# Optimization experiments

Measured on AMD Instinct MI355X. Metric: run time of the kernel, lower is better.

## Reference

```python
import jax, jax.numpy as jnp
import numpy as np

NUM_ITERATIONS = 3
LN_EPS = 1e-5


def setup_inputs() -> dict:
    key = jax.random.key(0)
    ks = jax.random.split(key, 10)
    B, L, Lv, H = 8, 2048, 256, 1024
    s = 1.0 / np.sqrt(H)
    s2 = 1.0 / np.sqrt(2 * H)
    return {
        "text_feat": jax.random.normal(ks[0], (B, L, H), dtype=jnp.float32),
        "vision_feat": jax.random.normal(ks[1], (B, Lv, H), dtype=jnp.float32),
        "Wt": jax.random.uniform(ks[2], (H, H), jnp.float32, -s, s),
        "bt": jax.random.uniform(ks[3], (H,), jnp.float32, -s, s),
        "Wv": jax.random.uniform(ks[4], (H, H), jnp.float32, -s, s),
        "bv": jax.random.uniform(ks[5], (H,), jnp.float32, -s, s),
        "Wg": jax.random.uniform(ks[6], (H, 2 * H), jnp.float32, -s2, s2),
        "bg": jax.random.uniform(ks[7], (H,), jnp.float32, -s2, s2),
        "gamma": jnp.ones((H,), jnp.float32),
        "beta": jnp.zeros((H,), jnp.float32),
    }


def reference(text_feat, vision_feat, Wt, bt, Wv, bv, Wg, bg, gamma, beta):
    B, L, H = text_feat.shape
    # mean-pool vision over its sequence, broadcast over L
    vision_pooled = jnp.mean(vision_feat, axis=1, keepdims=True)          # [B,1,H]
    text_proj = jnp.einsum('blh,oh->blo', text_feat, Wt) + bt             # [B,L,H]
    vision_proj = jnp.einsum('bkh,oh->bko', vision_pooled, Wv) + bv       # [B,1,H]
    vision_proj = jnp.broadcast_to(vision_proj, (B, L, H))                # expand to [B,L,H]

    # agreement is loop-invariant in the original code; compute once
    agreement = jnp.sum(text_proj * vision_proj, axis=-1, keepdims=True)  # [B,L,1]

    coupling = jnp.zeros((B, L, 1), dtype=text_feat.dtype)
    fused = text_feat
    for _ in range(NUM_ITERATIONS):
        routing_weights = jax.nn.softmax(coupling, axis=1)                # softmax over L
        weighted_vision = routing_weights * vision_proj                   # [B,L,H]
        # gate = sigmoid(Linear(concat(text_proj, weighted_vision)))
        Wg_t, Wg_v = Wg[:, :H], Wg[:, H:]
        gate_pre = (jnp.einsum('blh,oh->blo', text_proj, Wg_t)
                    + jnp.einsum('blh,oh->blo', weighted_vision, Wg_v) + bg)
        gate = jax.nn.sigmoid(gate_pre)
        fused = text_feat + gate * weighted_vision
        coupling = coupling + agreement

    # LayerNorm over last dim (dropout is identity in eval)
    mu = jnp.mean(fused, axis=-1, keepdims=True)
    var = jnp.mean(jnp.square(fused - mu), axis=-1, keepdims=True)
    out = (fused - mu) / jnp.sqrt(var + LN_EPS) * gamma + beta
    return out
```

## Files before the change

### kernel.cpp

```cpp
#include <hip/hip_runtime.h>
#include <hip/hip_bf16.h>
#include <hip/hip_fp8.h>

typedef __bf16 bf16_t;
typedef bf16_t bf16x4 __attribute__((ext_vector_type(4)));
typedef bf16_t bf16x8 __attribute__((ext_vector_type(8)));
typedef float  f32x4  __attribute__((ext_vector_type(4)));

#define B_  8
#define L_  2048
#define H_  1024
#define LV_ 256

typedef const __attribute__((address_space(1))) void* gptr_as1;
typedef __attribute__((address_space(3))) void* lptr_as3;

__device__ __forceinline__ void gload_lds16(void* lds_base, const void* gsrc) {
  __builtin_amdgcn_global_load_lds((gptr_as1)gsrc, (lptr_as3)lds_base, 16, 0, 0);
}

__device__ __forceinline__ unsigned char to_fp8(float x) {
  return __hip_fp8_e4m3(x).__x;
}

__global__ __launch_bounds__(256) void prep1(const float* __restrict__ vf,
                                             const float* __restrict__ Wt,
                                             const float* __restrict__ Wg,
                                             const float* __restrict__ bt,
                                             const float* __restrict__ bg,
                                             float* __restrict__ pooled,
                                             bf16_t* __restrict__ WtT,
                                             float* __restrict__ cbb,
                                             float* __restrict__ u) {
  __shared__ __align__(16) char shm[16640];
  int bid = blockIdx.x;
  int t = threadIdx.x;
  if (bid < 64) {
    float* part = (float*)shm;
    int b = bid >> 3, hc = bid & 7;
    int h = hc * 128 + (t & 127);
    int kh = t >> 7;
    const float* p = vf + (long)b * (LV_ * H_) + (long)kh * 128 * H_ + h;
    float s = 0.f;
    #pragma unroll 4
    for (int k = 0; k < 128; ++k) s += p[k * H_];
    part[t] = s;
    __syncthreads();
    if (t < 128)
      pooled[b * H_ + hc * 128 + t] = (part[t] + part[t + 128]) * (1.f / 256.f);
  } else if (bid < 320) {
    float (*tile)[65] = (float(*)[65])shm;
    int lb = bid - 64;
    int hr = (lb >> 4) * 64;
    int ec = (lb & 15) * 64;
    int lr = t >> 4, lc = t & 15;
    #pragma unroll
    for (int rr = 0; rr < 4; ++rr) {
      int r = rr * 16 + lr;
      float4 v = *(const float4*)(Wt + (long)(hr + r) * H_ + ec + lc * 4);
      tile[r][lc * 4 + 0] = v.x; tile[r][lc * 4 + 1] = v.y;
      tile[r][lc * 4 + 2] = v.z; tile[r][lc * 4 + 3] = v.w;
    }
    __syncthreads();
    #pragma unroll
    for (int rr = 0; rr < 4; ++rr) {
      int er = rr * 16 + lr;
      bf16x4 o = { (bf16_t)tile[lc * 4 + 0][er], (bf16_t)tile[lc * 4 + 1][er],
                   (bf16_t)tile[lc * 4 + 2][er], (bf16_t)tile[lc * 4 + 3][er] };
      *(bf16x4*)(WtT + (long)(ec + er) * H_ + hr + lc * 4) = o;
    }
  } else if (bid < 576) {
    int lb = bid - 320;
    int wid = t >> 6, lane = t & 63;
    int o = lb * 4 + wid;
    const float* wr = Wg + (long)o * 2048;
    float acc = 0.f;
    for (int j = 0; j < 16; ++j) acc += wr[lane + 64 * j] * bt[lane + 64 * j];
    for (int off = 32; off; off >>= 1) acc += __shfl_down(acc, off);
    if (lane == 0) cbb[o] = acc + bg[o];
  } else {
    int z = bid - 576;
    *(float4*)(u + z * 1024 + t * 4) = (float4){0.f, 0.f, 0.f, 0.f};
  }
}

__global__ void matvec8(const float* __restrict__ W, int ldw, int woff,
                        const float* __restrict__ x,
                        const float* __restrict__ bias,
                        float* __restrict__ out) {
  int wid = threadIdx.x >> 6, lane = threadIdx.x & 63;
  int o = blockIdx.x * 4 + wid;
  const float* wr = W + (long)o * ldw + woff;
  float acc[B_];
  #pragma unroll
  for (int b = 0; b < B_; ++b) acc[b] = 0.f;
  for (int j = 0; j < 16; ++j) {
    float w = wr[lane + 64 * j];
    #pragma unroll
    for (int b = 0; b < B_; ++b) acc[b] += w * x[b * H_ + lane + 64 * j];
  }
  #pragma unroll
  for (int b = 0; b < B_; ++b)
    for (int off = 32; off; off >>= 1) acc[b] += __shfl_down(acc[b], off);
  if (lane == 0) {
    float bb = bias ? bias[o] : 0.f;
    #pragma unroll
    for (int b = 0; b < B_; ++b) out[b * H_ + o] = acc[b] + bb;
  }
}

__global__ __launch_bounds__(256) void prep3(const float* __restrict__ Wg,
                                             const float* __restrict__ Wt,
                                             const float* __restrict__ vp,
                                             float* __restrict__ gv,
                                             float* __restrict__ u) {
  int bid = blockIdx.x;
  int t = threadIdx.x;
  if (bid < 256) {
    int wid = t >> 6, lane = t & 63;
    int o = bid * 4 + wid;
    const float* wr = Wg + (long)o * 2048 + 1024;
    float acc[B_];
    #pragma unroll
    for (int b = 0; b < B_; ++b) acc[b] = 0.f;
    for (int j = 0; j < 16; ++j) {
      float w = wr[lane + 64 * j];
      #pragma unroll
      for (int b = 0; b < B_; ++b) acc[b] += w * vp[b * H_ + lane + 64 * j];
    }
    #pragma unroll
    for (int b = 0; b < B_; ++b)
      for (int off = 32; off; off >>= 1) acc[b] += __shfl_down(acc[b], off);
    if (lane == 0) {
      #pragma unroll
      for (int b = 0; b < B_; ++b) gv[b * H_ + o] = acc[b];
    }
  } else {
    int lb = bid - 256;
    int e = (lb & 3) * 256 + t;
    int oc = lb >> 2;
    float a[B_];
    #pragma unroll
    for (int b = 0; b < B_; ++b) a[b] = 0.f;
    #pragma unroll
    for (int i = 0; i < 16; ++i) {
      int o = oc * 16 + i;
      float w = Wt[(long)o * H_ + e];
      #pragma unroll
      for (int b = 0; b < B_; ++b) a[b] += w * vp[b * H_ + o];
    }
    #pragma unroll
    for (int b = 0; b < B_; ++b) atomicAdd(u + b * 1024 + e, a[b]);
  }
}

__global__ __launch_bounds__(256) void cvt_wc(const float* __restrict__ text,
                                              const float* __restrict__ u,
                                              const float* __restrict__ Wg,
                                              const bf16_t* __restrict__ Bt,
                                              unsigned char* __restrict__ t8p,
                                              float* __restrict__ agr,
                                              unsigned char* __restrict__ Cw8) {
  __shared__ __align__(16) char shm[32800];
  int bid = blockIdx.x;
  int t = threadIdx.x;
  if (bid < 1024) {
    unsigned char (*q8)[1032] = (unsigned char(*)[1032])shm;
    float (*dred)[16] = (float(*)[16])(shm + 16512);
    int b = bid >> 7;
    int wid = t >> 6, lane = t & 63;
    const float4* trow = (const float4*)(text + (long)bid * (16 * H_));
    float4 uu = ((const float4*)(u + b * H_))[t];
    #pragma unroll 4
    for (int i = 0; i < 16; ++i) {
      float4 v = trow[i * 256 + t];
      float d = v.x * uu.x + v.y * uu.y + v.z * uu.z + v.w * uu.w;
      for (int off = 32; off; off >>= 1) d += __shfl_down(d, off);
      if (!lane) dred[wid][i] = d;
      uchar4 q = { to_fp8(v.x), to_fp8(v.y), to_fp8(v.z), to_fp8(v.w) };
      *(uchar4*)&q8[i][t * 4] = q;
    }
    __syncthreads();
    if (t < 16)
      agr[bid * 16 + t] = dred[0][t] + dred[1][t] + dred[2][t] + dred[3][t];
    unsigned char* dst = t8p + (long)(bid >> 2) * 65536 + (bid & 3) * 512;
    #pragma unroll
    for (int c = 0; c < 8; ++c) {
      int kb = wid * 8 + c;
      uint2 r = *(const uint2*)&q8[lane & 15][kb * 32 + (lane >> 4) * 8];
      *(uint2*)(dst + kb * 2048 + lane * 8) = r;
    }
    return;
  }
  const int tid = t;
  const int wid = tid >> 6, lane = tid & 63;
  const int fr = lane & 15, fkb = (lane >> 4) * 16, fq = (lane >> 4) * 4;
  const int wm = wid >> 1, wn = wid & 1;
  const int lb = bid - 1024;
  const int tm = lb & 15, tn = lb >> 4;
  const int m0 = tm * 64, n0 = tn * 64;

  char* ldsA = shm;

  const int d0 = tid * 16;
  const int p  = d0 ^ (((d0 >> 7) & 7) << 4);
  const int rS = p >> 7, cS = (p & 127) >> 1;

  const int swz = (fr & 7) << 4;
  const int e0 = fkb ^ swz;
  const int e1 = (64 + fkb) ^ swz;

  auto stage = [&](int tt) {
    char* base = ldsA + (tt & 1) * 16384;
    gload_lds16(base + 8192 + d0,        Bt + (long)(n0 + rS) * H_ + tt * 64 + cS);
    gload_lds16(base + 8192 + 4096 + d0, Bt + (long)(n0 + 32 + rS) * H_ + tt * 64 + cS);
    const float* a0 = Wg + (long)(m0 + rS) * 2048 + tt * 64 + cS;
    const float* a1 = Wg + (long)(m0 + 32 + rS) * 2048 + tt * 64 + cS;
    float4 x0 = *(const float4*)a0, x1 = *(const float4*)(a0 + 4);
    float4 y0 = *(const float4*)a1, y1 = *(const float4*)(a1 + 4);
    bf16x8 bx = { (bf16_t)x0.x, (bf16_t)x0.y, (bf16_t)x0.z, (bf16_t)x0.w,
                  (bf16_t)x1.x, (bf16_t)x1.y, (bf16_t)x1.z, (bf16_t)x1.w };
    bf16x8 by = { (bf16_t)y0.x, (bf16_t)y0.y, (bf16_t)y0.z, (bf16_t)y0.w,
                  (bf16_t)y1.x, (bf16_t)y1.y, (bf16_t)y1.z, (bf16_t)y1.w };
    *(bf16x8*)(base + d0) = bx;
    *(bf16x8*)(base + 4096 + d0) = by;
  };

  f32x4 acc[2][2];
  #pragma unroll
  for (int m = 0; m < 2; ++m)
    #pragma unroll
    for (int n = 0; n < 2; ++n) acc[m][n] = (f32x4){0.f, 0.f, 0.f, 0.f};

  stage(0);
  __syncthreads();
  for (int tt = 0; tt < 16; ++tt) {
    if (tt + 1 < 16) stage(tt + 1);
    char* buf = ldsA + (tt & 1) * 16384;
    char* AR = buf + (wm * 32 + fr) * 128;
    char* BR = buf + 8192 + (wn * 32 + fr) * 128;
    bf16x8 a[2][2], b[2][2];
    #pragma unroll
    for (int m = 0; m < 2; ++m) {
      a[m][0] = *(const bf16x8*)(AR + m * 2048 + e0);
      a[m][1] = *(const bf16x8*)(AR + m * 2048 + e1);
      b[m][0] = *(const bf16x8*)(BR + m * 2048 + e0);
      b[m][1] = *(const bf16x8*)(BR + m * 2048 + e1);
    }
    #pragma unroll
    for (int m = 0; m < 2; ++m)
      #pragma unroll
      for (int n = 0; n < 2; ++n) {
        acc[m][n] = __builtin_amdgcn_mfma_f32_16x16x32_bf16(a[m][0], b[n][0], acc[m][n], 0, 0, 0);
        acc[m][n] = __builtin_amdgcn_mfma_f32_16x16x32_bf16(a[m][1], b[n][1], acc[m][n], 0, 0, 0);
      }
    __syncthreads();
  }
  #pragma unroll
  for (int m = 0; m < 2; ++m)
    #pragma unroll
    for (int r_ = 0; r_ < 4; ++r_) {
      int row = m0 + wm * 32 + m * 16 + fq + r_;
      #pragma unroll
      for (int n = 0; n < 2; ++n) {
        int col = n0 + wn * 32 + n * 16 + fr;
        Cw8[(long)(row >> 7) * 131072 + (col >> 5) * 4096 + ((row >> 4) & 7) * 512
            + ((row & 15) + (((col >> 3) & 3) << 4)) * 8 + (col & 7)]
          = to_fp8(acc[m][n][r_] * 16.f);
      }
    }
}

#define BOFF 16777216
__global__ __launch_bounds__(512, 2)
void gemm_ln(const unsigned char* __restrict__ AB,
             const float* __restrict__ textf,
             const float* __restrict__ cbb, const float* __restrict__ agrb,
             const float* __restrict__ gvb, const float* __restrict__ vpb,
             const float* __restrict__ gamma, const float* __restrict__ beta,
             float* __restrict__ out) {
  extern __shared__ __align__(16) char dlds[];
  const int tid  = threadIdx.x;
  const int w    = tid >> 6;
  const int lane = tid & 63;
  const int fr   = lane & 15;
  const int fq   = (lane >> 4) * 4;
  const int bid  = blockIdx.x;
  const long m0  = (long)bid * 64;
  const int bat  = (int)(m0 >> 11);

  {
    float* red = (float*)(dlds + 118784);
    float* rvA = (float*)(dlds + 118848);
    float4 av = *(const float4*)(agrb + (long)bat * 2048 + tid * 4);
    float mloc = fmaxf(fmaxf(av.x, av.y), fmaxf(av.z, av.w)) * 2.f;
    #pragma unroll
    for (int off = 32; off; off >>= 1) mloc = fmaxf(mloc, __shfl_xor(mloc, off));
    if ((tid & 63) == 0) red[tid >> 6] = mloc;
    __syncthreads();
    float mx = red[0];
    #pragma unroll
    for (int i = 1; i < 8; ++i) mx = fmaxf(mx, red[i]);
    float sl = __expf(2.f * av.x - mx) + __expf(2.f * av.y - mx)
             + __expf(2.f * av.z - mx) + __expf(2.f * av.w - mx);
    #pragma unroll
    for (int off = 32; off; off >>= 1) sl += __shfl_xor(sl, off);
    __syncthreads();
    if ((tid & 63) == 0) red[tid >> 6] = sl;
    __syncthreads();
    float ssum = red[0] + red[1] + red[2] + red[3]
               + red[4] + red[5] + red[6] + red[7];
    if (tid < 64) rvA[tid] = __expf(2.f * agrb[m0 + tid] - mx) / ssum;
    __syncthreads();
  }

  {
    char* P = dlds + 98304;
    if (tid < 256) {
      gload_lds16(P + tid * 16,          cbb + tid * 4);
      gload_lds16(P + 8192 + tid * 16,   vpb + bat * H_ + tid * 4);
      gload_lds16(P + 16384 + tid * 16,  beta + tid * 4);
    } else {
      int t2 = tid - 256;
      gload_lds16(P + 4096 + t2 * 16,    gvb + bat * H_ + t2 * 4);
      gload_lds16(P + 12288 + t2 * 16,   gamma + t2 * 4);
    }
  }

  const unsigned char* aSrc = AB + (long)bid * 65536 + lane * 16;
  const unsigned char* bSrc = AB + BOFF + (long)w * 131072 + lane * 16;
  char* const wBase = dlds + w * 12288;

  f32x4 acc[4][8];
  #pragma unroll
  for (int m = 0; m < 4; ++m)
    #pragma unroll
    for (int n = 0; n < 8; ++n) acc[m][n] = (f32x4){0.f, 0.f, 0.f, 0.f};

#define STAGE(t)                                                        \
  {                                                                     \
    char* D_ = wBase + ((t) & 1) * 6144 + lane * 16;                    \
    const unsigned char* As_ = aSrc + (t) * 2048;                       \
    gload_lds16(D_,        As_);                                        \
    gload_lds16(D_ + 1024, As_ + 1024);                                 \
    const unsigned char* Bs_ = bSrc + (t) * 4096;                       \
    _Pragma("unroll")                                                   \
    for (int r_ = 0; r_ < 4; ++r_)                                      \
      gload_lds16(D_ + 2048 + r_ * 1024, Bs_ + r_ * 1024);              \
  }
#define KITER(t, WN)                                                    \
  {                                                                     \
    asm volatile("s_waitcnt lgkmcnt(0)" ::: "memory");                  \
    __builtin_amdgcn_sched_barrier(0);                                  \
    if ((t) + 1 < 32) STAGE((t) + 1)                                    \
    asm volatile("s_waitcnt vmcnt(" #WN ")" ::: "memory");              \
    __builtin_amdgcn_sched_barrier(0);                                  \
    const char* R_ = wBase + ((t) & 1) * 6144 + lane * 8;               \
    long a_[4], b_[8];                                                  \
    _Pragma("unroll")                                                   \
    for (int m_ = 0; m_ < 4; ++m_)                                      \
      a_[m_] = *(const long*)(R_ + m_ * 512);                           \
    _Pragma("unroll")                                                   \
    for (int n_ = 0; n_ < 8; ++n_)                                      \
      b_[n_] = *(const long*)(R_ + 2048 + n_ * 512);                    \
    _Pragma("unroll")                                                   \
    for (int m_ = 0; m_ < 4; ++m_)                                      \
      _Pragma("unroll")                                                 \
      for (int n_ = 0; n_ < 8; ++n_)                                    \
        acc[m_][n_] = __builtin_amdgcn_mfma_f32_16x16x32_fp8_fp8(       \
            a_[m_], b_[n_], acc[m_][n_], 0, 0, 0);                      \
  }

  STAGE(0)

  KITER(0, 6)  KITER(1, 6)  KITER(2, 6)  KITER(3, 6)
  KITER(4, 6)  KITER(5, 6)  KITER(6, 6)  KITER(7, 6)
  KITER(8, 6)  KITER(9, 6)  KITER(10, 6) KITER(11, 6)
  KITER(12, 6) KITER(13, 6) KITER(14, 6) KITER(15, 6)
  KITER(16, 6) KITER(17, 6) KITER(18, 6) KITER(19, 6)
  KITER(20, 6) KITER(21, 6) KITER(22, 6) KITER(23, 6)
  KITER(24, 6) KITER(25, 6) KITER(26, 6) KITER(27, 6)
  KITER(28, 6) KITER(29, 6) KITER(30, 6) KITER(31, 0)
#undef KITER
#undef STAGE

  const int lr = tid >> 5;
  const int jj = tid & 31;
  char* P = dlds + 98304;
  const float* rvA = (const float*)(dlds + 118848);

  #pragma unroll
  for (int m = 0; m < 4; ++m) {
    __syncthreads();
    #pragma unroll
    for (int n = 0; n < 8; ++n) {
      #pragma unroll
      for (int r = 0; r < 4; ++r) {
        int rl = fq + r;
        int c  = (w * 128 + n * 16 + fr) ^ (((rl >> 2) & 3) << 4);
        *(float*)(dlds + rl * 4096 + c * 4) = acc[m][n][r];
      }
    }
    __syncthreads();
    long row = m0 + m * 16 + lr;
    float rv = rvA[m * 16 + lr];
    const float* tf = textf + row * H_;
    const int rot = ((lr >> 2) & 3) << 4;
    float s = 0.f, q = 0.f;
    #pragma unroll 2
    for (int k = 0; k < 8; ++k) {
      int c0 = k * 128 + jj * 4;
      char* slot = dlds + lr * 4096 + ((c0 ^ rot) * 4);
      f32x4 a4 = *(const f32x4*)slot;
      float4 t4  = *(const float4*)(tf + c0);
      f32x4 cb4 = *(const f32x4*)(P + c0 * 4);
      f32x4 gv4 = *(const f32x4*)(P + 4096 + c0 * 4);
      f32x4 vp4 = *(const f32x4*)(P + 8192 + c0 * 4);
      f32x4 f4;
      float gp, g;
      gp = a4[0] * 0.0625f + cb4[0] + rv * gv4[0];
      g = 1.f / (1.f + __expf(-gp));
      f4[0] = t4.x + g * rv * vp4[0];
      gp = a4[1] * 0.0625f + cb4[1] + rv * gv4[1];
      g = 1.f / (1.f + __expf(-gp));
      f4[1] = t4.y + g * rv * vp4[1];
      gp = a4[2] * 0.0625f + cb4[2] + rv * gv4[2];
      g = 1.f / (1.f + __expf(-gp));
      f4[2] = t4.z + g * rv * vp4[2];
      gp = a4[3] * 0.0625f + cb4[3] + rv * gv4[3];
      g = 1.f / (1.f + __expf(-gp));
      f4[3] = t4.w + g * rv * vp4[3];
      *(f32x4*)slot = f4;
      s += f4[0] + f4[1] + f4[2] + f4[3];
      q += f4[0] * f4[0] + f4[1] * f4[1] + f4[2] * f4[2] + f4[3] * f4[3];
    }
    #pragma unroll
    for (int off = 1; off < 32; off <<= 1) {
      s += __shfl_xor(s, off);
      q += __shfl_xor(q, off);
    }
    float mu  = s * (1.f / H_);
    float var = q * (1.f / H_) - mu * mu;
    float inv = rsqrtf(var + 1e-5f);
    float* op = out + row * H_;
    #pragma unroll 2
    for (int k = 0; k < 8; ++k) {
      int c0 = k * 128 + jj * 4;
      f32x4 f4 = *(const f32x4*)(dlds + lr * 4096 + ((c0 ^ rot) * 4));
      f32x4 gg = *(const f32x4*)(P + 12288 + c0 * 4);
      f32x4 bb = *(const f32x4*)(P + 16384 + c0 * 4);
      float4 o4;
      o4.x = (f4[0] - mu) * inv * gg[0] + bb[0];
      o4.y = (f4[1] - mu) * inv * gg[1] + bb[1];
      o4.z = (f4[2] - mu) * inv * gg[2] + bb[2];
      o4.w = (f4[3] - mu) * inv * gg[3] + bb[3];
      *(float4*)(op + c0) = o4;
    }
  }
}

extern "C" void kernel_launch(void* const* d_in, const int* in_sizes, int n_in,
                              void* d_out, int out_size, void* d_ws, size_t ws_size,
                              hipStream_t stream) {
  const float* text  = (const float*)d_in[0];
  const float* vis   = (const float*)d_in[1];
  const float* Wt    = (const float*)d_in[2];
  const float* bt    = (const float*)d_in[3];
  const float* Wv    = (const float*)d_in[4];
  const float* bv    = (const float*)d_in[5];
  const float* Wg    = (const float*)d_in[6];
  const float* bg    = (const float*)d_in[7];
  const float* gamma = (const float*)d_in[8];
  const float* beta  = (const float*)d_in[9];
  float* out = (float*)d_out;

  char* ws = (char*)d_ws;
  unsigned char* t8p   = (unsigned char*)(ws);
  unsigned char* Wc8p  = (unsigned char*)(ws + (size_t)16777216);
  bf16_t* WtT_b = (bf16_t*)(ws + (size_t)17825792);
  float*  pooled = (float*)(ws + (size_t)19922944);
  float*  vp     = (float*)(ws + (size_t)19955712);
  float*  gv     = (float*)(ws + (size_t)19988480);
  float*  u      = (float*)(ws + (size_t)20021248);
  float*  cbb    = (float*)(ws + (size_t)20054016);
  float*  agr    = (float*)(ws + (size_t)20123648);

  static bool smem_set = false;
  if (!smem_set) {
    (void)hipFuncSetAttribute((const void*)gemm_ln,
                              hipFuncAttributeMaxDynamicSharedMemorySize, 119296);
    smem_set = true;
  }

  prep1<<<584, 256, 0, stream>>>(vis, Wt, Wg, bt, bg, pooled, WtT_b, cbb, u);
  matvec8<<<256, 256, 0, stream>>>(Wv, 1024, 0, pooled, bv, vp);
  prep3<<<512, 256, 0, stream>>>(Wg, Wt, vp, gv, u);
  cvt_wc<<<1280, 256, 0, stream>>>(text, u, Wg, WtT_b, t8p, agr, Wc8p);
  gemm_ln<<<256, 512, 119296, stream>>>(t8p, text, cbb, agr, gv, vp,
                                        gamma, beta, out);
}
```

Baseline: 98.89 us.

## Merge four prep kernels into one persistent kernel with grid barriers

New measurement: 313.1 us. 3.17x slower.

```diff
diff --git a/kernel.cpp b/kernel.cpp
--- a/kernel.cpp
+++ b/kernel.cpp
@@ -23,18 +23,33 @@
   return __hip_fp8_e4m3(x).__x;
 }
 
-__global__ __launch_bounds__(256) void prep1(const float* __restrict__ vf,
-                                             const float* __restrict__ Wt,
-                                             const float* __restrict__ Wg,
-                                             const float* __restrict__ bt,
-                                             const float* __restrict__ bg,
-                                             float* __restrict__ pooled,
-                                             bf16_t* __restrict__ WtT,
-                                             float* __restrict__ cbb,
-                                             float* __restrict__ u) {
-  __shared__ __align__(16) char shm[16640];
-  int bid = blockIdx.x;
-  int t = threadIdx.x;
+__device__ __forceinline__ void grid_bar(unsigned int* bar, unsigned int target) {
+  __syncthreads();
+  if (threadIdx.x == 0) {
+    __threadfence();
+    atomicAdd(bar, 1u);
+    while (__hip_atomic_load(bar, __ATOMIC_RELAXED, __HIP_MEMORY_SCOPE_AGENT)
+           < target)
+      __builtin_amdgcn_s_sleep(8);
+    __threadfence();
+  }
+  __syncthreads();
+}
+
+__global__ __launch_bounds__(256, 4)
+void mega_prep(const float* __restrict__ vf, const float* __restrict__ Wt,
+               const float* __restrict__ Wg, const float* __restrict__ bt,
+               const float* __restrict__ bg, const float* __restrict__ bv,
+               const float* __restrict__ Wv, const float* __restrict__ text,
+               float* __restrict__ pooled, bf16_t* __restrict__ WtT,
+               float* __restrict__ cbb, float* __restrict__ u,
+               float* __restrict__ vp, float* __restrict__ gv,
+               unsigned char* __restrict__ t8p, float* __restrict__ agr,
+               unsigned char* __restrict__ Cw8, unsigned int* __restrict__ bar) {
+  __shared__ __align__(16) char shm[33024];
+  const int bid = blockIdx.x;
+  const int t = threadIdx.x;
+
   if (bid < 64) {
     float* part = (float*)shm;
     int b = bid >> 3, hc = bid & 7;
@@ -78,44 +93,35 @@
     for (int j = 0; j < 16; ++j) acc += wr[lane + 64 * j] * bt[lane + 64 * j];
     for (int off = 32; off; off >>= 1) acc += __shfl_down(acc, off);
     if (lane == 0) cbb[o] = acc + bg[o];
-  } else {
+  } else if (bid < 584) {
     int z = bid - 576;
     *(float4*)(u + z * 1024 + t * 4) = (float4){0.f, 0.f, 0.f, 0.f};
   }
-}
-
-__global__ void matvec8(const float* __restrict__ W, int ldw, int woff,
-                        const float* __restrict__ x,
-                        const float* __restrict__ bias,
-                        float* __restrict__ out) {
-  int wid = threadIdx.x >> 6, lane = threadIdx.x & 63;
-  int o = blockIdx.x * 4 + wid;
-  const float* wr = W + (long)o * ldw + woff;
-  float acc[B_];
-  #pragma unroll
-  for (int b = 0; b < B_; ++b) acc[b] = 0.f;
-  for (int j = 0; j < 16; ++j) {
-    float w = wr[lane + 64 * j];
-    #pragma unroll
-    for (int b = 0; b < B_; ++b) acc[b] += w * x[b * H_ + lane + 64 * j];
-  }
-  #pragma unroll
-  for (int b = 0; b < B_; ++b)
-    for (int off = 32; off; off >>= 1) acc[b] += __shfl_down(acc[b], off);
-  if (lane == 0) {
-    float bb = bias ? bias[o] : 0.f;
-    #pragma unroll
-    for (int b = 0; b < B_; ++b) out[b * H_ + o] = acc[b] + bb;
-  }
-}
-
-__global__ __launch_bounds__(256) void prep3(const float* __restrict__ Wg,
-                                             const float* __restrict__ Wt,
-                                             const float* __restrict__ vp,
-                                             float* __restrict__ gv,
-                                             float* __restrict__ u) {
-  int bid = blockIdx.x;
-  int t = threadIdx.x;
+  grid_bar(bar, 768);
+
+  if (bid < 256) {
+    int wid = t >> 6, lane = t & 63;
+    int o = bid * 4 + wid;
+    const float* wr = Wv + (long)o * H_;
+    float acc[B_];
+    #pragma unroll
+    for (int b = 0; b < B_; ++b) acc[b] = 0.f;
+    for (int j = 0; j < 16; ++j) {
+      float w = wr[lane + 64 * j];
+      #pragma unroll
+      for (int b = 0; b < B_; ++b) acc[b] += w * pooled[b * H_ + lane + 64 * j];
+    }
+    #pragma unroll
+    for (int b = 0; b < B_; ++b)
+      for (int off = 32; off; off >>= 1) acc[b] += __shfl_down(acc[b], off);
+    if (lane == 0) {
+      float bb = bv[o];
+      #pragma unroll
+      for (int b = 0; b < B_; ++b) vp[b * H_ + o] = acc[b] + bb;
+    }
+  }
+  grid_bar(bar, 1536);
+
   if (bid < 256) {
     int wid = t >> 6, lane = t & 63;
     int o = bid * 4 + wid;
@@ -135,7 +141,7 @@
       #pragma unroll
       for (int b = 0; b < B_; ++b) gv[b * H_ + o] = acc[b];
     }
-  } else {
+  } else if (bid < 512) {
     int lb = bid - 256;
     int e = (lb & 3) * 256 + t;
     int oc = lb >> 2;
@@ -152,123 +158,115 @@
     #pragma unroll
     for (int b = 0; b < B_; ++b) atomicAdd(u + b * 1024 + e, a[b]);
   }
-}
-
-__global__ __launch_bounds__(256) void cvt_wc(const float* __restrict__ text,
-                                              const float* __restrict__ u,
-                                              const float* __restrict__ Wg,
-                                              const bf16_t* __restrict__ Bt,
-                                              unsigned char* __restrict__ t8p,
-                                              float* __restrict__ agr,
-                                              unsigned char* __restrict__ Cw8) {
-  __shared__ __align__(16) char shm[32800];
-  int bid = blockIdx.x;
-  int t = threadIdx.x;
-  if (bid < 1024) {
-    unsigned char (*q8)[1032] = (unsigned char(*)[1032])shm;
-    float (*dred)[16] = (float(*)[16])(shm + 16512);
-    int b = bid >> 7;
-    int wid = t >> 6, lane = t & 63;
-    const float4* trow = (const float4*)(text + (long)bid * (16 * H_));
-    float4 uu = ((const float4*)(u + b * H_))[t];
-    #pragma unroll 4
-    for (int i = 0; i < 16; ++i) {
-      float4 v = trow[i * 256 + t];
-      float d = v.x * uu.x + v.y * uu.y + v.z * uu.z + v.w * uu.w;
-      for (int off = 32; off; off >>= 1) d += __shfl_down(d, off);
-      if (!lane) dred[wid][i] = d;
-      uchar4 q = { to_fp8(v.x), to_fp8(v.y), to_fp8(v.z), to_fp8(v.w) };
-      *(uchar4*)&q8[i][t * 4] = q;
-    }
-    __syncthreads();
-    if (t < 16)
-      agr[bid * 16 + t] = dred[0][t] + dred[1][t] + dred[2][t] + dred[3][t];
-    unsigned char* dst = t8p + (long)(bid >> 2) * 65536 + (bid & 3) * 512;
-    #pragma unroll
-    for (int c = 0; c < 8; ++c) {
-      int kb = wid * 8 + c;
-      uint2 r = *(const uint2*)&q8[lane & 15][kb * 32 + (lane >> 4) * 8];
-      *(uint2*)(dst + kb * 2048 + lane * 8) = r;
-    }
-    return;
-  }
-  const int tid = t;
-  const int wid = tid >> 6, lane = tid & 63;
-  const int fr = lane & 15, fkb = (lane >> 4) * 16, fq = (lane >> 4) * 4;
-  const int wm = wid >> 1, wn = wid & 1;
-  const int lb = bid - 1024;
-  const int tm = lb & 15, tn = lb >> 4;
-  const int m0 = tm * 64, n0 = tn * 64;
-
-  char* ldsA = shm;
-
-  const int d0 = tid * 16;
-  const int p  = d0 ^ (((d0 >> 7) & 7) << 4);
-  const int rS = p >> 7, cS = (p & 127) >> 1;
-
-  const int swz = (fr & 7) << 4;
-  const int e0 = fkb ^ swz;
-  const int e1 = (64 + fkb) ^ swz;
-
-  auto stage = [&](int tt) {
-    char* base = ldsA + (tt & 1) * 16384;
-    gload_lds16(base + 8192 + d0,        Bt + (long)(n0 + rS) * H_ + tt * 64 + cS);
-    gload_lds16(base + 8192 + 4096 + d0, Bt + (long)(n0 + 32 + rS) * H_ + tt * 64 + cS);
-    const float* a0 = Wg + (long)(m0 + rS) * 2048 + tt * 64 + cS;
-    const float* a1 = Wg + (long)(m0 + 32 + rS) * 2048 + tt * 64 + cS;
-    float4 x0 = *(const float4*)a0, x1 = *(const float4*)(a0 + 4);
-    float4 y0 = *(const float4*)a1, y1 = *(const float4*)(a1 + 4);
-    bf16x8 bx = { (bf16_t)x0.x, (bf16_t)x0.y, (bf16_t)x0.z, (bf16_t)x0.w,
-                  (bf16_t)x1.x, (bf16_t)x1.y, (bf16_t)x1.z, (bf16_t)x1.w };
-    bf16x8 by = { (bf16_t)y0.x, (bf16_t)y0.y, (bf16_t)y0.z, (bf16_t)y0.w,
-                  (bf16_t)y1.x, (bf16_t)y1.y, (bf16_t)y1.z, (bf16_t)y1.w };
-    *(bf16x8*)(base + d0) = bx;
-    *(bf16x8*)(base + 4096 + d0) = by;
-  };
-
-  f32x4 acc[2][2];
-  #pragma unroll
-  for (int m = 0; m < 2; ++m)
-    #pragma unroll
-    for (int n = 0; n < 2; ++n) acc[m][n] = (f32x4){0.f, 0.f, 0.f, 0.f};
-
-  stage(0);
-  __syncthreads();
-  for (int tt = 0; tt < 16; ++tt) {
-    if (tt + 1 < 16) stage(tt + 1);
-    char* buf = ldsA + (tt & 1) * 16384;
-    char* AR = buf + (wm * 32 + fr) * 128;
-    char* BR = buf + 8192 + (wn * 32 + fr) * 128;
-    bf16x8 a[2][2], b[2][2];
-    #pragma unroll
-    for (int m = 0; m < 2; ++m) {
-      a[m][0] = *(const bf16x8*)(AR + m * 2048 + e0);
-      a[m][1] = *(const bf16x8*)(AR + m * 2048 + e1);
-      b[m][0] = *(const bf16x8*)(BR + m * 2048 + e0);
-      b[m][1] = *(const bf16x8*)(BR + m * 2048 + e1);
-    }
-    #pragma unroll
-    for (int m = 0; m < 2; ++m)
-      #pragma unroll
-      for (int n = 0; n < 2; ++n) {
-        acc[m][n] = __builtin_amdgcn_mfma_f32_16x16x32_bf16(a[m][0], b[n][0], acc[m][n], 0, 0, 0);
-        acc[m][n] = __builtin_amdgcn_mfma_f32_16x16x32_bf16(a[m][1], b[n][1], acc[m][n], 0, 0, 0);
+  grid_bar(bar, 2304);
+
+  for (int u_ = bid; u_ < 1280; u_ += 768) {
+    if (u_ < 256) {
+      const int tid = t;
+      const int wid = tid >> 6, lane = tid & 63;
+      const int fr = lane & 15, fkb = (lane >> 4) * 16, fq = (lane >> 4) * 4;
+      const int wm = wid >> 1, wn = wid & 1;
+      const int tm = u_ & 15, tn = u_ >> 4;
+      const int m0 = tm * 64, n0 = tn * 64;
+      char* ldsA = shm;
+      const int d0 = tid * 16;
+      const int p  = d0 ^ (((d0 >> 7) & 7) << 4);
+      const int rS = p >> 7, cS = (p & 127) >> 1;
+      const int swz = (fr & 7) << 4;
+      const int e0 = fkb ^ swz;
+      const int e1 = (64 + fkb) ^ swz;
+
+      auto stage = [&](int tt) {
+        char* base = ldsA + (tt & 1) * 16384;
+        gload_lds16(base + 8192 + d0,        WtT + (long)(n0 + rS) * H_ + tt * 64 + cS);
+        gload_lds16(base + 8192 + 4096 + d0, WtT + (long)(n0 + 32 + rS) * H_ + tt * 64 + cS);
+        const float* a0 = Wg + (long)(m0 + rS) * 2048 + tt * 64 + cS;
+        const float* a1 = Wg + (long)(m0 + 32 + rS) * 2048 + tt * 64 + cS;
+        float4 x0 = *(const float4*)a0, x1 = *(const float4*)(a0 + 4);
+        float4 y0 = *(const float4*)a1, y1 = *(const float4*)(a1 + 4);
+        bf16x8 bx = { (bf16_t)x0.x, (bf16_t)x0.y, (bf16_t)x0.z, (bf16_t)x0.w,
+                      (bf16_t)x1.x, (bf16_t)x1.y, (bf16_t)x1.z, (bf16_t)x1.w };
+        bf16x8 by = { (bf16_t)y0.x, (bf16_t)y0.y, (bf16_t)y0.z, (bf16_t)y0.w,
+                      (bf16_t)y1.x, (bf16_t)y1.y, (bf16_t)y1.z, (bf16_t)y1.w };
+        *(bf16x8*)(base + d0) = bx;
+        *(bf16x8*)(base + 4096 + d0) = by;
+      };
+
+      f32x4 acc[2][2];
+      #pragma unroll
+      for (int m = 0; m < 2; ++m)
+        #pragma unroll
+        for (int n = 0; n < 2; ++n) acc[m][n] = (f32x4){0.f, 0.f, 0.f, 0.f};
+
+      stage(0);
+      __syncthreads();
+      for (int tt = 0; tt < 16; ++tt) {
+        if (tt + 1 < 16) stage(tt + 1);
+        char* buf = ldsA + (tt & 1) * 16384;
+        char* AR = buf + (wm * 32 + fr) * 128;
+        char* BR = buf + 8192 + (wn * 32 + fr) * 128;
+        bf16x8 a[2][2], b[2][2];
+        #pragma unroll
+        for (int m = 0; m < 2; ++m) {
+          a[m][0] = *(const bf16x8*)(AR + m * 2048 + e0);
+          a[m][1] = *(const bf16x8*)(AR + m * 2048 + e1);
+          b[m][0] = *(const bf16x8*)(BR + m * 2048 + e0);
+          b[m][1] = *(const bf16x8*)(BR + m * 2048 + e1);
+        }
+        #pragma unroll
+        for (int m = 0; m < 2; ++m)
+          #pragma unroll
+          for (int n = 0; n < 2; ++n) {
+            acc[m][n] = __builtin_amdgcn_mfma_f32_16x16x32_bf16(a[m][0], b[n][0], acc[m][n], 0, 0, 0);
+            acc[m][n] = __builtin_amdgcn_mfma_f32_16x16x32_bf16(a[m][1], b[n][1], acc[m][n], 0, 0, 0);
+          }
+        __syncthreads();
       }
-    __syncthreads();
-  }
-  #pragma unroll
-  for (int m = 0; m < 2; ++m)
-    #pragma unroll
-    for (int r_ = 0; r_ < 4; ++r_) {
-      int row = m0 + wm * 32 + m * 16 + fq + r_;
-      #pragma unroll
-      for (int n = 0; n < 2; ++n) {
-        int col = n0 + wn * 32 + n * 16 + fr;
-        Cw8[(long)(row >> 7) * 131072 + (col >> 5) * 4096 + ((row >> 4) & 7) * 512
-            + ((row & 15) + (((col >> 3) & 3) << 4)) * 8 + (col & 7)]
-          = to_fp8(acc[m][n][r_] * 16.f);
+      #pragma unroll
+      for (int m = 0; m < 2; ++m)
+        #pragma unroll
+        for (int r_ = 0; r_ < 4; ++r_) {
+          int row = m0 + wm * 32 + m * 16 + fq + r_;
+          #pragma unroll
+          for (int n = 0; n < 2; ++n) {
+            int col = n0 + wn * 32 + n * 16 + fr;
+            Cw8[(long)(row >> 7) * 131072 + (col >> 5) * 4096 + ((row >> 4) & 7) * 512
+                + ((row & 15) + (((col >> 3) & 3) << 4)) * 8 + (col & 7)]
+              = to_fp8(acc[m][n][r_] * 16.f);
+          }
+        }
+      __syncthreads();
+    } else {
+      int pb = u_ - 256;
+      unsigned char (*q8)[1032] = (unsigned char(*)[1032])shm;
+      float (*dred)[16] = (float(*)[16])(shm + 16512);
+      int b = pb >> 7;
+      int wid = t >> 6, lane = t & 63;
+      const float4* trow = (const float4*)(text + (long)pb * (16 * H_));
+      float4 uu = ((const float4*)(u + b * H_))[t];
+      __syncthreads();
+      #pragma unroll 4
+      for (int i = 0; i < 16; ++i) {
+        float4 v = trow[i * 256 + t];
+        float d = v.x * uu.x + v.y * uu.y + v.z * uu.z + v.w * uu.w;
+        for (int off = 32; off; off >>= 1) d += __shfl_down(d, off);
+        if (!lane) dred[wid][i] = d;
+        uchar4 q = { to_fp8(v.x), to_fp8(v.y), to_fp8(v.z), to_fp8(v.w) };
+        *(uchar4*)&q8[i][t * 4] = q;
       }
-    }
+      __syncthreads();
+      if (t < 16)
+        agr[pb * 16 + t] = dred[0][t] + dred[1][t] + dred[2][t] + dred[3][t];
+      unsigned char* dst = t8p + (long)(pb >> 2) * 65536 + (pb & 3) * 512;
+      #pragma unroll
+      for (int c = 0; c < 8; ++c) {
+        int kb = wid * 8 + c;
+        uint2 r = *(const uint2*)&q8[lane & 15][kb * 32 + (lane >> 4) * 8];
+        *(uint2*)(dst + kb * 2048 + lane * 8) = r;
+      }
+      __syncthreads();
+    }
+  }
 }
 
 #define BOFF 16777216
@@ -484,6 +482,7 @@
   float*  u      = (float*)(ws + (size_t)20021248);
   float*  cbb    = (float*)(ws + (size_t)20054016);
   float*  agr    = (float*)(ws + (size_t)20123648);
+  unsigned int* bar = (unsigned int*)(ws + (size_t)20189184);
 
   static bool smem_set = false;
   if (!smem_set) {
@@ -492,10 +491,10 @@
     smem_set = true;
   }
 
-  prep1<<<584, 256, 0, stream>>>(vis, Wt, Wg, bt, bg, pooled, WtT_b, cbb, u);
-  matvec8<<<256, 256, 0, stream>>>(Wv, 1024, 0, pooled, bv, vp);
-  prep3<<<512, 256, 0, stream>>>(Wg, Wt, vp, gv, u);
-  cvt_wc<<<1280, 256, 0, stream>>>(text, u, Wg, WtT_b, t8p, agr, Wc8p);
+  hipMemsetAsync(bar, 0, 4, stream);
+  mega_prep<<<768, 256, 0, stream>>>(vis, Wt, Wg, bt, bg, bv, Wv, text,
+                                     pooled, WtT_b, cbb, u, vp, gv,
+                                     t8p, agr, Wc8p, bar);
   gemm_ln<<<256, 512, 119296, stream>>>(t8p, text, cbb, agr, gv, vp,
                                         gamma, beta, out);
 }
```

## Move text fp8 quantization into prep1 and compute agreement from fp8 copy

Applied to the files above, without the earlier changes.

After: 97.19 us. About the same (-1.7%).

```diff
diff --git a/kernel.cpp b/kernel.cpp
--- a/kernel.cpp
+++ b/kernel.cpp
@@ -21,6 +21,9 @@
 
 __device__ __forceinline__ unsigned char to_fp8(float x) {
   return __hip_fp8_e4m3(x).__x;
+}
+__device__ __forceinline__ float from_fp8(unsigned char b) {
+  __hip_fp8_e4m3 v; v.__x = b; return (float)v;
 }
 
 __global__ __launch_bounds__(256) void prep1(const float* __restrict__ vf,
@@ -28,10 +31,12 @@
                                              const float* __restrict__ Wg,
                                              const float* __restrict__ bt,
                                              const float* __restrict__ bg,
+                                             const float* __restrict__ text,
                                              float* __restrict__ pooled,
                                              bf16_t* __restrict__ WtT,
                                              float* __restrict__ cbb,
-                                             float* __restrict__ u) {
+                                             float* __restrict__ u,
+                                             unsigned char* __restrict__ t8p) {
   __shared__ __align__(16) char shm[16640];
   int bid = blockIdx.x;
   int t = threadIdx.x;
@@ -78,9 +83,28 @@
     for (int j = 0; j < 16; ++j) acc += wr[lane + 64 * j] * bt[lane + 64 * j];
     for (int off = 32; off; off >>= 1) acc += __shfl_down(acc, off);
     if (lane == 0) cbb[o] = acc + bg[o];
-  } else {
+  } else if (bid < 584) {
     int z = bid - 576;
     *(float4*)(u + z * 1024 + t * 4) = (float4){0.f, 0.f, 0.f, 0.f};
+  } else {
+    int pb = bid - 584;
+    unsigned char (*q8)[1032] = (unsigned char(*)[1032])shm;
+    int wid = t >> 6, lane = t & 63;
+    const float4* trow = (const float4*)(text + (long)pb * (16 * H_));
+    #pragma unroll 4
+    for (int i = 0; i < 16; ++i) {
+      float4 v = trow[i * 256 + t];
+      uchar4 qq = { to_fp8(v.x), to_fp8(v.y), to_fp8(v.z), to_fp8(v.w) };
+      *(uchar4*)&q8[i][t * 4] = qq;
+    }
+    __syncthreads();
+    unsigned char* dst = t8p + (long)(pb >> 2) * 65536 + (pb & 3) * 512;
+    #pragma unroll
+    for (int c = 0; c < 8; ++c) {
+      int kb = wid * 8 + c;
+      uint2 r = *(const uint2*)&q8[lane & 15][kb * 32 + (lane >> 4) * 8];
+      *(uint2*)(dst + kb * 2048 + lane * 8) = r;
+    }
   }
 }
 
@@ -154,49 +178,45 @@
   }
 }
 
-__global__ __launch_bounds__(256) void cvt_wc(const float* __restrict__ text,
-                                              const float* __restrict__ u,
-                                              const float* __restrict__ Wg,
-                                              const bf16_t* __restrict__ Bt,
-                                              unsigned char* __restrict__ t8p,
-                                              float* __restrict__ agr,
-                                              unsigned char* __restrict__ Cw8) {
+__global__ __launch_bounds__(256) void agwc(const unsigned char* __restrict__ t8p,
+                                            const float* __restrict__ u,
+                                            const float* __restrict__ Wg,
+                                            const bf16_t* __restrict__ Bt,
+                                            float* __restrict__ agr,
+                                            unsigned char* __restrict__ Cw8) {
   __shared__ __align__(16) char shm[32800];
   int bid = blockIdx.x;
   int t = threadIdx.x;
-  if (bid < 1024) {
-    unsigned char (*q8)[1032] = (unsigned char(*)[1032])shm;
-    float (*dred)[16] = (float(*)[16])(shm + 16512);
-    int b = bid >> 7;
-    int wid = t >> 6, lane = t & 63;
-    const float4* trow = (const float4*)(text + (long)bid * (16 * H_));
-    float4 uu = ((const float4*)(u + b * H_))[t];
+  if (bid < 256) {
+    float* uL = (float*)shm;
+    int b = bid >> 5;
+    ((float4*)uL)[t] = ((const float4*)(u + b * 1024))[t];
+    __syncthreads();
+    int mb_l = t >> 6, li = t & 63;
+    int row = li & 15, p = li >> 4;
+    const unsigned char* src = t8p + (long)bid * 65536 + mb_l * 512 + li * 8;
+    float s = 0.f;
     #pragma unroll 4
-    for (int i = 0; i < 16; ++i) {
-      float4 v = trow[i * 256 + t];
-      float d = v.x * uu.x + v.y * uu.y + v.z * uu.z + v.w * uu.w;
-      for (int off = 32; off; off >>= 1) d += __shfl_down(d, off);
-      if (!lane) dred[wid][i] = d;
-      uchar4 q = { to_fp8(v.x), to_fp8(v.y), to_fp8(v.z), to_fp8(v.w) };
-      *(uchar4*)&q8[i][t * 4] = q;
-    }
-    __syncthreads();
-    if (t < 16)
-      agr[bid * 16 + t] = dred[0][t] + dred[1][t] + dred[2][t] + dred[3][t];
-    unsigned char* dst = t8p + (long)(bid >> 2) * 65536 + (bid & 3) * 512;
-    #pragma unroll
-    for (int c = 0; c < 8; ++c) {
-      int kb = wid * 8 + c;
-      uint2 r = *(const uint2*)&q8[lane & 15][kb * 32 + (lane >> 4) * 8];
-      *(uint2*)(dst + kb * 2048 + lane * 8) = r;
-    }
+    for (int kb = 0; kb < 32; ++kb) {
+      uint2 d = *(const uint2*)(src + kb * 2048);
+      const float* up = uL + kb * 32 + p * 8;
+      #pragma unroll
+      for (int j = 0; j < 4; ++j)
+        s += from_fp8((unsigned char)(d.x >> (8 * j))) * up[j];
+      #pragma unroll
+      for (int j = 0; j < 4; ++j)
+        s += from_fp8((unsigned char)(d.y >> (8 * j))) * up[4 + j];
+    }
+    s += __shfl_xor(s, 16);
+    s += __shfl_xor(s, 32);
+    if (p == 0) agr[(long)bid * 64 + mb_l * 16 + row] = s;
     return;
   }
   const int tid = t;
   const int wid = tid >> 6, lane = tid & 63;
   const int fr = lane & 15, fkb = (lane >> 4) * 16, fq = (lane >> 4) * 4;
   const int wm = wid >> 1, wn = wid & 1;
-  const int lb = bid - 1024;
+  const int lb = bid - 256;
   const int tm = lb & 15, tn = lb >> 4;
   const int m0 = tm * 64, n0 = tn * 64;
 
@@ -492,10 +512,11 @@
     smem_set = true;
   }
 
-  prep1<<<584, 256, 0, stream>>>(vis, Wt, Wg, bt, bg, pooled, WtT_b, cbb, u);
+  prep1<<<1608, 256, 0, stream>>>(vis, Wt, Wg, bt, bg, text,
+                                  pooled, WtT_b, cbb, u, t8p);
   matvec8<<<256, 256, 0, stream>>>(Wv, 1024, 0, pooled, bv, vp);
   prep3<<<512, 256, 0, stream>>>(Wg, Wt, vp, gv, u);
-  cvt_wc<<<1280, 256, 0, stream>>>(text, u, Wg, WtT_b, t8p, agr, Wc8p);
+  agwc<<<512, 256, 0, stream>>>(t8p, u, Wg, WtT_b, agr, Wc8p);
   gemm_ln<<<256, 512, 119296, stream>>>(t8p, text, cbb, agr, gv, vp,
                                         gamma, beta, out);
 }
```
